# Optimization experiments

Measured on AMD Instinct MI355X. Metric: run time of the kernel, lower is better.

## Reference

```python
import jax, jax.numpy as jnp
import numpy as np

N_NODES = 100000
N_EDGES = 1600000


def gcn_conv(h_in, src, dst, norm, W, b, n_nodes):
    # h_in: [N, Fin]; src/dst: [E'] (self-loops included); norm: [E']
    h = h_in @ W                                    # [N, Fout]
    msg = h[src] * norm[:, None]                    # gather + scale
    out = jax.ops.segment_sum(msg, dst, num_segments=n_nodes)
    return out + b


def _with_self_loops_and_norm(edge_index, n_nodes):
    loop = jnp.arange(n_nodes, dtype=edge_index.dtype)
    src = jnp.concatenate([edge_index[0], loop])
    dst = jnp.concatenate([edge_index[1], loop])
    deg = jax.ops.segment_sum(jnp.ones_like(dst, dtype=jnp.float32), dst,
                              num_segments=n_nodes)
    dinv = jnp.where(deg > 0, jax.lax.rsqrt(deg), 0.0)
    norm = dinv[src] * dinv[dst]                    # [E+N]
    return src, dst, norm


def setup_inputs() -> dict:
    key = jax.random.key(0)
    k1, k2, k3, k4 = jax.random.split(key, 4)
    x = jax.random.normal(k1, (N_NODES, 256), dtype=jnp.float32)
    edge_index = jax.random.randint(k2, (2, N_EDGES), 0, N_NODES, dtype=jnp.int64)
    W1 = jax.random.normal(k3, (256, 128), dtype=jnp.float32) * (1.0 / np.sqrt(256))
    b1 = jnp.zeros((128,), dtype=jnp.float32)
    W2 = jax.random.normal(k4, (128, 40), dtype=jnp.float32) * (1.0 / np.sqrt(128))
    b2 = jnp.zeros((40,), dtype=jnp.float32)
    return {"x": x, "edge_index": edge_index, "W1": W1, "b1": b1, "W2": W2, "b2": b2}


def reference(x, edge_index, W1, b1, W2, b2):
    n_nodes = x.shape[0]
    src, dst, norm = _with_self_loops_and_norm(edge_index, n_nodes)
    h = jax.nn.relu(gcn_conv(x, src, dst, norm, W1, b1, n_nodes))
    # dropout p=0.5 is identity in eval mode
    h = gcn_conv(h, src, dst, norm, W2, b2, n_nodes)
    return jax.nn.log_softmax(h, axis=-1)
```

## Files before the change

kernel.cpp:

```cpp
#include <hip/hip_runtime.h>
#include <hip/hip_bf16.h>
#include <math.h>

#define FIN 256
#define FMID 128
#define FOUT 40

typedef __attribute__((ext_vector_type(8))) short bf16x8;
typedef __attribute__((ext_vector_type(4))) float f32x4;

__device__ __forceinline__ short f2b(float f) {
    __hip_bfloat16 h = __float2bfloat16(f);
    return *reinterpret_cast<short*>(&h);
}

__device__ __forceinline__ float blo(uint b) { union { uint u; float f; } v; v.u = b << 16; return v.f; }
__device__ __forceinline__ float bhi(uint b) { union { uint u; float f; } v; v.u = b & 0xFFFF0000u; return v.f; }

__global__ __launch_bounds__(256) void k_initcounts(int* counts, int n) {
    int i = blockIdx.x * 256 + threadIdx.x;
    if (i < n) counts[i] = 1;
}

__global__ __launch_bounds__(256) void k_count(const int* __restrict__ dst,
                                               int* __restrict__ counts, int E) {
    int e = blockIdx.x * 256 + threadIdx.x;
    if (e < E) atomicAdd(&counts[dst[e]], 1);
}

__global__ __launch_bounds__(256) void k_alloc(const int* __restrict__ counts,
                                               int* __restrict__ start,
                                               float* __restrict__ dinv,
                                               int* __restrict__ gcnt, int n) {
    __shared__ int s[256];
    __shared__ int base_s;
    int t = threadIdx.x;
    int i = blockIdx.x * 256 + t;
    int c = (i < n) ? counts[i] : 0;
    s[t] = c;
    __syncthreads();
    #pragma unroll
    for (int off = 1; off < 256; off <<= 1) {
        int v = (t >= off) ? s[t - off] : 0;
        __syncthreads();
        s[t] += v;
        __syncthreads();
    }
    if (t == 255) base_s = atomicAdd(gcnt, s[255]);
    __syncthreads();
    if (i < n) {
        start[i] = base_s + s[t] - c;
        dinv[i]  = rsqrtf((float)c);
    }
}

__global__ __launch_bounds__(256) void k_fill(const int* __restrict__ src,
                                              const int* __restrict__ dst,
                                              const int* __restrict__ start,
                                              int* __restrict__ cursor,
                                              int* __restrict__ ebuf, int E, int Nn) {
    int tid = blockIdx.x * 256 + threadIdx.x;
    if (tid >= E + Nn) return;
    int s, d;
    if (tid < E) { s = src[tid]; d = dst[tid]; }
    else         { s = tid - E;  d = s; }
    int pos = atomicAdd(&cursor[d], 1);
    ebuf[start[d] + pos] = s;
}

__global__ __launch_bounds__(256) void k_prepw1(const float* __restrict__ W1,
                                                short* __restrict__ w1t) {
    int t = blockIdx.x * 256 + threadIdx.x;
    if (t >= FIN * FMID) return;
    int k = t >> 7;
    int n = t & 127;
    w1t[n * FIN + k] = f2b(W1[t]);
}

__global__ __launch_bounds__(256) void k_gemm1b(const float* __restrict__ A,
                                                const short* __restrict__ w1t,
                                                ushort* __restrict__ Cb, int M) {
    __shared__ short Bs[FMID * FIN];

    const int t = threadIdx.x;
    {
        int c  = t & 31;
        int r0 = t >> 5;
        #pragma unroll
        for (int p = 0; p < 16; ++p) {
            int n = r0 + p * 8;
            int dst = n * FIN + ((c * 8) ^ ((n & 7) << 3));
            *(bf16x8*)(&Bs[dst]) = *(const bf16x8*)(&w1t[n * FIN + c * 8]);
        }
    }
    __syncthreads();

    const int wid  = t >> 6;
    const int lane = t & 63;
    const int l15  = lane & 15;
    const int kg   = lane >> 4;
    const int mbase = blockIdx.x * 128 + wid * 32;

    f32x4 acc[2][8] = {};

    for (int ks = 0; ks < 8; ++ks) {
        const int k0 = ks * 32;
        bf16x8 bf[8];
        #pragma unroll
        for (int ct = 0; ct < 8; ++ct) {
            int n = ct * 16 + l15;
            bf[ct] = *(const bf16x8*)(&Bs[n * FIN + ((k0 + kg * 8) ^ ((n & 7) << 3))]);
        }
        #pragma unroll
        for (int rt = 0; rt < 2; ++rt) {
            int row = mbase + rt * 16 + l15;
            bf16x8 af = {0, 0, 0, 0, 0, 0, 0, 0};
            if (row < M) {
                const float* ap = &A[(size_t)row * FIN + k0 + kg * 8];
                float4 a0 = *(const float4*)(ap);
                float4 a1 = *(const float4*)(ap + 4);
                af[0] = f2b(a0.x); af[1] = f2b(a0.y);
                af[2] = f2b(a0.z); af[3] = f2b(a0.w);
                af[4] = f2b(a1.x); af[5] = f2b(a1.y);
                af[6] = f2b(a1.z); af[7] = f2b(a1.w);
            }
            #pragma unroll
            for (int ct = 0; ct < 8; ++ct)
                acc[rt][ct] = __builtin_amdgcn_mfma_f32_16x16x32_bf16(
                    af, bf[ct], acc[rt][ct], 0, 0, 0);
        }
    }

    #pragma unroll
    for (int rt = 0; rt < 2; ++rt) {
        #pragma unroll
        for (int r = 0; r < 4; ++r) {
            int row = mbase + rt * 16 + kg * 4 + r;
            if (row < M) {
                #pragma unroll
                for (int ct = 0; ct < 8; ++ct)
                    Cb[(size_t)row * FMID + ct * 16 + l15] =
                        (ushort)f2b(acc[rt][ct][r]);
            }
        }
    }
}

__global__ __launch_bounds__(256) void k_agg1(const ushort* __restrict__ hb,
                                              const int* __restrict__ ebuf,
                                              const int* __restrict__ start,
                                              const int* __restrict__ cnt,
                                              const float* __restrict__ dinv,
                                              const float* __restrict__ b1,
                                              float* __restrict__ out, int Nn) {
    int node = __builtin_amdgcn_readfirstlane(blockIdx.x * 4 + (threadIdx.x >> 6));
    int lane = threadIdx.x & 63;
    if (node >= Nn) return;
    int rs = start[node];
    int n  = cnt[node];
    float di = dinv[node];
    float2 acc = make_float2(0.f, 0.f);
    const int off2 = lane * 2;
    int k = 0;
    for (; k + 4 <= n; k += 4) {
        int s0 = ebuf[rs + k + 0];
        int s1 = ebuf[rs + k + 1];
        int s2 = ebuf[rs + k + 2];
        int s3 = ebuf[rs + k + 3];
        float w0 = dinv[s0], w1 = dinv[s1], w2 = dinv[s2], w3 = dinv[s3];
        uint v0 = *(const uint*)(&hb[(size_t)s0 * FMID + off2]);
        uint v1 = *(const uint*)(&hb[(size_t)s1 * FMID + off2]);
        uint v2 = *(const uint*)(&hb[(size_t)s2 * FMID + off2]);
        uint v3 = *(const uint*)(&hb[(size_t)s3 * FMID + off2]);
        acc.x += w0 * blo(v0) + w1 * blo(v1) + w2 * blo(v2) + w3 * blo(v3);
        acc.y += w0 * bhi(v0) + w1 * bhi(v1) + w2 * bhi(v2) + w3 * bhi(v3);
    }
    for (; k < n; ++k) {
        int s   = ebuf[rs + k];
        float w = dinv[s];
        uint v  = *(const uint*)(&hb[(size_t)s * FMID + off2]);
        acc.x += w * blo(v);
        acc.y += w * bhi(v);
    }
    float2 bv = *(const float2*)(&b1[off2]);
    acc.x = fmaxf(di * acc.x + bv.x, 0.f);
    acc.y = fmaxf(di * acc.y + bv.y, 0.f);
    *(float2*)(&out[(size_t)node * FMID + off2]) = acc;
}

#define G2_PAD 132
__global__ __launch_bounds__(256) void k_gemm2(const float* __restrict__ A,
                                               const float* __restrict__ W2,
                                               float* __restrict__ C, int M) {
    __shared__ float w2s[FMID * FOUT];
    __shared__ float As[64 * G2_PAD];

    const int t = threadIdx.x;
    const int block_row = blockIdx.x * 64;

    for (int idx = t; idx < FMID * FOUT; idx += 256) w2s[idx] = W2[idx];

    {
        int r  = t >> 5;
        int c4 = (t & 31) * 4;
        #pragma unroll
        for (int p = 0; p < 8; ++p) {
            int row = block_row + r + p * 8;
            float4 v = (row < M) ? *(const float4*)(&A[(size_t)row * FMID + c4])
                                 : make_float4(0.f, 0.f, 0.f, 0.f);
            *(float4*)(&As[(r + p * 8) * G2_PAD + c4]) = v;
        }
    }
    __syncthreads();

    const int cg    = t & 7;
    const int rg    = t >> 3;
    const int cbase = cg * 5;
    const float* a0p = &As[(rg * 2 + 0) * G2_PAD];
    const float* a1p = &As[(rg * 2 + 1) * G2_PAD];

    float acc0[5] = {}, acc1[5] = {};
    #pragma unroll 4
    for (int k = 0; k < FMID; ++k) {
        float a0 = a0p[k];
        float a1 = a1p[k];
        #pragma unroll
        for (int j = 0; j < 5; ++j) {
            float w = w2s[k * FOUT + cbase + j];
            acc0[j] += a0 * w;
            acc1[j] += a1 * w;
        }
    }

    int row0 = block_row + rg * 2;
    if (row0 < M) {
        #pragma unroll
        for (int j = 0; j < 5; ++j) C[(size_t)row0 * FOUT + cbase + j] = acc0[j];
    }
    if (row0 + 1 < M) {
        #pragma unroll
        for (int j = 0; j < 5; ++j) C[(size_t)(row0 + 1) * FOUT + cbase + j] = acc1[j];
    }
}

__global__ __launch_bounds__(256) void k_agg2(const float* __restrict__ h,
                                              const int* __restrict__ ebuf,
                                              const int* __restrict__ start,
                                              const int* __restrict__ cnt,
                                              const float* __restrict__ dinv,
                                              const float* __restrict__ b2,
                                              float* __restrict__ out, int Nn) {
    int node = __builtin_amdgcn_readfirstlane(blockIdx.x * 4 + (threadIdx.x >> 6));
    int lane = threadIdx.x & 63;
    if (node >= Nn) return;
    int rs = start[node];
    int n  = cnt[node];
    float di = dinv[node];
    float acc = 0.f;
    bool active = (lane < FOUT);
    int lidx = active ? lane : 0;
    int k = 0;
    for (; k + 4 <= n; k += 4) {
        int s0 = ebuf[rs + k + 0];
        int s1 = ebuf[rs + k + 1];
        int s2 = ebuf[rs + k + 2];
        int s3 = ebuf[rs + k + 3];
        float w0 = dinv[s0], w1 = dinv[s1], w2 = dinv[s2], w3 = dinv[s3];
        float v0 = h[(size_t)s0 * FOUT + lidx];
        float v1 = h[(size_t)s1 * FOUT + lidx];
        float v2 = h[(size_t)s2 * FOUT + lidx];
        float v3 = h[(size_t)s3 * FOUT + lidx];
        acc += w0 * v0 + w1 * v1 + w2 * v2 + w3 * v3;
    }
    for (; k < n; ++k) {
        int s   = ebuf[rs + k];
        acc += dinv[s] * h[(size_t)s * FOUT + lidx];
    }
    float v = active ? di * acc + b2[lane] : -INFINITY;
    float m = v;
    #pragma unroll
    for (int off = 32; off >= 1; off >>= 1) m = fmaxf(m, __shfl_xor(m, off));
    float e = active ? expf(v - m) : 0.f;
    float ssum = e;
    #pragma unroll
    for (int off = 32; off >= 1; off >>= 1) ssum += __shfl_xor(ssum, off);
    if (active) out[(size_t)node * FOUT + lane] = v - m - logf(ssum);
}

extern "C" void kernel_launch(void* const* d_in, const int* in_sizes, int n_in,
                              void* d_out, int out_size, void* d_ws, size_t ws_size,
                              hipStream_t stream) {
    const float* x  = (const float*)d_in[0];
    const int*   ei = (const int*)d_in[1];
    const float* W1 = (const float*)d_in[2];
    const float* b1 = (const float*)d_in[3];
    const float* W2 = (const float*)d_in[4];
    const float* b2 = (const float*)d_in[5];

    const int N = in_sizes[0] / FIN;
    const int E = in_sizes[1] / 2;
    float* out = (float*)d_out;

    ushort* h1b   = (ushort*)d_ws;
    float*  agg1  = (float*)(h1b + (size_t)N * FMID);
    float*  dinv  = agg1 + (size_t)N * FMID;
    int*    counts= (int*)(dinv + N);
    int*    start = counts + N;
    int*    gcnt  = start + N;
    int*    ebuf  = gcnt + 64;
    short*  w1t   = (short*)(ebuf + (size_t)(E + N));
    float*  h2    = (float*)h1b;

    const int* srcp = ei;
    const int* dstp = ei + E;
    const int  EN   = E + N;

    k_prepw1<<<(FIN * FMID + 255) / 256, 256, 0, stream>>>(W1, w1t);

    hipMemsetAsync(gcnt, 0, sizeof(int), stream);
    k_initcounts<<<(N + 255) / 256, 256, 0, stream>>>(counts, N);
    k_count     <<<(E + 255) / 256, 256, 0, stream>>>(dstp, counts, E);
    k_alloc     <<<(N + 255) / 256, 256, 0, stream>>>(counts, start, dinv, gcnt, N);
    hipMemsetAsync(counts, 0, (size_t)N * sizeof(int), stream);
    k_fill      <<<(EN + 255) / 256, 256, 0, stream>>>(srcp, dstp, start, counts, ebuf, E, N);

    k_gemm1b<<<(N + 127) / 128, 256, 0, stream>>>(x, w1t, h1b, N);
    k_agg1  <<<(N + 3) / 4, 256, 0, stream>>>(h1b, ebuf, start, counts, dinv, b1, agg1, N);

    k_gemm2<<<(N + 63) / 64, 256, 0, stream>>>(agg1, W2, h2, N);
    k_agg2 <<<(N + 3) / 4, 256, 0, stream>>>(h2, ebuf, start, counts, dinv, b2, out, N);
}
```

Before: 521.9 us.

## Record edge slot during counting to remove second atomic pass; transpose W2 for vector loads

The CSR build now captures each edge's slot from the counting atomicAdd, so the fill pass writes directly without a second round of atomics. The init-counts kernel is dropped in favour of a memset, and self-loops are placed by the allocation kernel. Separately, gemm2 stores W2 transposed in shared memory so both operands can be read with float4 loads. The cost is an extra E-sized position buffer in the workspace plus the traffic to write and re-read it.

```diff
diff --git a/kernel.cpp b/kernel.cpp
--- a/kernel.cpp
+++ b/kernel.cpp
@@ -17,26 +17,23 @@
 __device__ __forceinline__ float blo(uint b) { union { uint u; float f; } v; v.u = b << 16; return v.f; }
 __device__ __forceinline__ float bhi(uint b) { union { uint u; float f; } v; v.u = b & 0xFFFF0000u; return v.f; }
 
-__global__ __launch_bounds__(256) void k_initcounts(int* counts, int n) {
-    int i = blockIdx.x * 256 + threadIdx.x;
-    if (i < n) counts[i] = 1;
-}
-
-__global__ __launch_bounds__(256) void k_count(const int* __restrict__ dst,
-                                               int* __restrict__ counts, int E) {
+__global__ __launch_bounds__(256) void k_count_pos(const int* __restrict__ dst,
+                                                   int* __restrict__ counts,
+                                                   int* __restrict__ pos, int E) {
     int e = blockIdx.x * 256 + threadIdx.x;
-    if (e < E) atomicAdd(&counts[dst[e]], 1);
-}
-
-__global__ __launch_bounds__(256) void k_alloc(const int* __restrict__ counts,
+    if (e < E) pos[e] = atomicAdd(&counts[dst[e]], 1);
+}
+
+__global__ __launch_bounds__(256) void k_alloc(int* __restrict__ counts,
                                                int* __restrict__ start,
                                                float* __restrict__ dinv,
-                                               int* __restrict__ gcnt, int n) {
+                                               int* __restrict__ gcnt,
+                                               int* __restrict__ ebuf, int n) {
     __shared__ int s[256];
     __shared__ int base_s;
     int t = threadIdx.x;
     int i = blockIdx.x * 256 + t;
-    int c = (i < n) ? counts[i] : 0;
+    int c = (i < n) ? counts[i] + 1 : 0;
     s[t] = c;
     __syncthreads();
     #pragma unroll
@@ -49,23 +46,23 @@
     if (t == 255) base_s = atomicAdd(gcnt, s[255]);
     __syncthreads();
     if (i < n) {
-        start[i] = base_s + s[t] - c;
-        dinv[i]  = rsqrtf((float)c);
-    }
-}
-
-__global__ __launch_bounds__(256) void k_fill(const int* __restrict__ src,
-                                              const int* __restrict__ dst,
-                                              const int* __restrict__ start,
-                                              int* __restrict__ cursor,
-                                              int* __restrict__ ebuf, int E, int Nn) {
-    int tid = blockIdx.x * 256 + threadIdx.x;
-    if (tid >= E + Nn) return;
-    int s, d;
-    if (tid < E) { s = src[tid]; d = dst[tid]; }
-    else         { s = tid - E;  d = s; }
-    int pos = atomicAdd(&cursor[d], 1);
-    ebuf[start[d] + pos] = s;
+        int st = base_s + s[t] - c;
+        start[i]  = st;
+        dinv[i]   = rsqrtf((float)c);
+        counts[i] = c;
+        ebuf[st]  = i;
+    }
+}
+
+__global__ __launch_bounds__(256) void k_fill2(const int* __restrict__ src,
+                                               const int* __restrict__ dst,
+                                               const int* __restrict__ start,
+                                               const int* __restrict__ pos,
+                                               int* __restrict__ ebuf, int E) {
+    int e = blockIdx.x * 256 + threadIdx.x;
+    if (e >= E) return;
+    int d = dst[e];
+    ebuf[start[d] + 1 + pos[e]] = src[e];
 }
 
 __global__ __launch_bounds__(256) void k_prepw1(const float* __restrict__ W1,
@@ -192,13 +189,17 @@
 __global__ __launch_bounds__(256) void k_gemm2(const float* __restrict__ A,
                                                const float* __restrict__ W2,
                                                float* __restrict__ C, int M) {
-    __shared__ float w2s[FMID * FOUT];
+    __shared__ float w2t[FOUT * G2_PAD];
     __shared__ float As[64 * G2_PAD];
 
     const int t = threadIdx.x;
     const int block_row = blockIdx.x * 64;
 
-    for (int idx = t; idx < FMID * FOUT; idx += 256) w2s[idx] = W2[idx];
+    for (int idx = t; idx < FMID * FOUT; idx += 256) {
+        int k = idx / FOUT;
+        int j = idx - k * FOUT;
+        w2t[j * G2_PAD + k] = W2[idx];
+    }
 
     {
         int r  = t >> 5;
@@ -221,14 +222,14 @@
 
     float acc0[5] = {}, acc1[5] = {};
     #pragma unroll 4
-    for (int k = 0; k < FMID; ++k) {
-        float a0 = a0p[k];
-        float a1 = a1p[k];
+    for (int k = 0; k < FMID; k += 4) {
+        float4 a0 = *(const float4*)(a0p + k);
+        float4 a1 = *(const float4*)(a1p + k);
         #pragma unroll
         for (int j = 0; j < 5; ++j) {
-            float w = w2s[k * FOUT + cbase + j];
-            acc0[j] += a0 * w;
-            acc1[j] += a1 * w;
+            float4 w = *(const float4*)(&w2t[(cbase + j) * G2_PAD + k]);
+            acc0[j] += a0.x * w.x + a0.y * w.y + a0.z * w.z + a0.w * w.w;
+            acc1[j] += a1.x * w.x + a1.y * w.y + a1.z * w.z + a1.w * w.w;
         }
     }
 
@@ -309,20 +310,19 @@
     int*    gcnt  = start + N;
     int*    ebuf  = gcnt + 64;
     short*  w1t   = (short*)(ebuf + (size_t)(E + N));
+    int*    pos   = (int*)(w1t + FIN * FMID);
     float*  h2    = (float*)h1b;
 
     const int* srcp = ei;
     const int* dstp = ei + E;
-    const int  EN   = E + N;
 
     k_prepw1<<<(FIN * FMID + 255) / 256, 256, 0, stream>>>(W1, w1t);
 
     hipMemsetAsync(gcnt, 0, sizeof(int), stream);
-    k_initcounts<<<(N + 255) / 256, 256, 0, stream>>>(counts, N);
-    k_count     <<<(E + 255) / 256, 256, 0, stream>>>(dstp, counts, E);
-    k_alloc     <<<(N + 255) / 256, 256, 0, stream>>>(counts, start, dinv, gcnt, N);
     hipMemsetAsync(counts, 0, (size_t)N * sizeof(int), stream);
-    k_fill      <<<(EN + 255) / 256, 256, 0, stream>>>(srcp, dstp, start, counts, ebuf, E, N);
+    k_count_pos<<<(E + 255) / 256, 256, 0, stream>>>(dstp, counts, pos, E);
+    k_alloc    <<<(N + 255) / 256, 256, 0, stream>>>(counts, start, dinv, gcnt, ebuf, N);
+    k_fill2    <<<(E + 255) / 256, 256, 0, stream>>>(srcp, dstp, start, pos, ebuf, E);
 
     k_gemm1b<<<(N + 127) / 128, 256, 0, stream>>>(x, w1t, h1b, N);
     k_agg1  <<<(N + 3) / 4, 256, 0, stream>>>(h1b, ebuf, start, counts, dinv, b1, agg1, N);
```

Result: faster. 475.9 us (-8.8%).
